# Kernel tuning notes

Hardware: AMD Instinct MI355X
Metric: run time of the kernel (lower is better)

## Reference

```python
import jax, jax.numpy as jnp
import numpy as np

N, F, H, L, E, C = 50000, 256, 64, 8, 1600000, 40
ALPHA, THETA = 0.1, 0.5


def setup_inputs() -> dict:
    key = jax.random.key(0)
    ks = jax.random.split(key, 8)
    x = jax.random.normal(ks[0], (N, F), jnp.float32)
    edge_index = jax.random.randint(ks[1], (2, E), 0, N)
    edge_weight = jax.random.uniform(ks[2], (E,), jnp.float32)
    W0 = jax.random.normal(ks[3], (F, H), jnp.float32) / np.sqrt(F).astype(np.float32)
    b0 = jnp.zeros((H,), jnp.float32)
    Wl = jax.random.normal(ks[4], (L, H, H), jnp.float32) / np.sqrt(H).astype(np.float32)
    W2 = jax.random.normal(ks[5], (H * H, C), jnp.float32) / np.sqrt(H * H).astype(np.float32)
    b2 = jnp.zeros((C,), jnp.float32)
    return dict(x=x, edge_index=edge_index, edge_weight=edge_weight,
                W0=W0, b0=b0, Wl=Wl, W2=W2, b2=b2)


def reference(x, edge_index, edge_weight, W0, b0, Wl, W2, b2):
    src, dst = edge_index[0], edge_index[1]
    # initial projection (dropout p=0.0 is identity)
    h0 = jax.nn.relu(x @ W0 + b0)          # [N, H]
    h = h0
    for l in range(L):
        # GCN2Conv, shared_weights=True, normalize=False
        # SpMM: agg[dst] += w * h[src]
        agg = jax.ops.segment_sum(edge_weight[:, None] * h[src], dst, num_segments=N)
        beta = jnp.float32(np.log(THETA / (l + 1) + 1.0))
        hmix = (1.0 - ALPHA) * agg + ALPHA * h0  # initial residual blend
        h = jax.nn.relu((1.0 - beta) * hmix + beta * (hmix @ Wl[l]))
    # outer-product head: [N,H,H] -> [N, H*H]
    op = jnp.einsum('ni,nj->nij', h, h).reshape(N, H * H)
    logits = op @ W2 + b2                  # [N, C]
    return jax.nn.log_softmax(logits, axis=-1)
```

## Files before the change

kernel.cpp:

```cpp
#include <hip/hip_runtime.h>
#include <hip/hip_bf16.h>
#include <math.h>

#define NN 50000
#define FF 256
#define HH 64
#define LL 8
#define EE 1600000
#define CC 40

#define BK 64
#define NB ((NN + BK - 1) / BK)
#define PBK 4096
#define NPART ((EE + PBK - 1) / PBK)

using short8 = __attribute__((ext_vector_type(8))) short;
using short4v = __attribute__((ext_vector_type(4))) short;
using f32x4  = __attribute__((ext_vector_type(4))) float;

static __device__ __forceinline__ unsigned short f2b(float f) {
    union { __hip_bfloat16 h; unsigned short u; } cv;
    cv.h = __float2bfloat16(f);
    return cv.u;
}
static __device__ __forceinline__ float b2f(unsigned short u) {
    return __uint_as_float((unsigned)u << 16);
}


__global__ void k_hist(const int* __restrict__ dst, int* __restrict__ cnt) {
    int e = blockIdx.x * 256 + threadIdx.x;
    if (e < EE) atomicAdd(&cnt[dst[e]], 1);
}

__global__ void k_scanA(const int* __restrict__ cnt, int* __restrict__ incl, int* __restrict__ bsum) {
    __shared__ int buf[1024];
    int i = blockIdx.x * 1024 + threadIdx.x;
    int v = (i < NN) ? cnt[i] : 0;
    buf[threadIdx.x] = v;
    __syncthreads();
    for (int off = 1; off < 1024; off <<= 1) {
        int t = (threadIdx.x >= off) ? buf[threadIdx.x - off] : 0;
        __syncthreads();
        buf[threadIdx.x] += t;
        __syncthreads();
    }
    if (i < NN) incl[i] = buf[threadIdx.x];
    if (threadIdx.x == 1023) bsum[blockIdx.x] = buf[1023];
}

__global__ void k_scanB(int* __restrict__ bsum) {
    int t = threadIdx.x;
    int vin = (t < 49) ? bsum[t] : 0;
    int v = vin;
    for (int off = 1; off < 64; off <<= 1) {
        int u = __shfl_up(v, off);
        if (t >= off) v += u;
    }
    if (t < 49) bsum[t] = v - vin;
}

__global__ void k_scanC(const int* __restrict__ cnt, const int* __restrict__ incl,
                        const int* __restrict__ bsum, int* __restrict__ row_ptr) {
    int i = blockIdx.x * 1024 + threadIdx.x;
    if (i < NN) row_ptr[i] = incl[i] - cnt[i] + bsum[blockIdx.x];
    if (i == 0) row_ptr[NN] = EE;
}

__global__ void k_binit(const int* __restrict__ row_ptr, int* __restrict__ bcur) {
    int t = blockIdx.x * 256 + threadIdx.x;
    if (t < NB) bcur[t] = row_ptr[t * BK];
}

__global__ void k_part(const int* __restrict__ src, const int* __restrict__ dst,
                       const float* __restrict__ w, int* __restrict__ bcur,
                       uint2* __restrict__ ebuk) {
    __shared__ int lh[NB];
    __shared__ int lbase[NB];
    int t = threadIdx.x;
    int e0 = blockIdx.x * PBK;
    int e1 = min(e0 + PBK, EE);
    for (int i = t; i < NB; i += 256) lh[i] = 0;
    __syncthreads();
    for (int e = e0 + t; e < e1; e += 256)
        atomicAdd(&lh[(unsigned)dst[e] >> 6], 1);
    __syncthreads();
    for (int i = t; i < NB; i += 256) {
        int c = lh[i];
        lbase[i] = c ? atomicAdd(&bcur[i], c) : 0;
    }
    __syncthreads();
    for (int i = t; i < NB; i += 256) lh[i] = 0;
    __syncthreads();
    for (int e = e0 + t; e < e1; e += 256) {
        int d = dst[e];
        int b = (unsigned)d >> 6;
        int r = atomicAdd(&lh[b], 1);
        ebuk[lbase[b] + r] = make_uint2(((unsigned)src[e] << 16) | (unsigned)f2b(w[e]),
                                        (unsigned)d);
    }
}

__global__ void k_sub(const int* __restrict__ row_ptr, const uint2* __restrict__ ebuk,
                      unsigned* __restrict__ pay) {
    __shared__ int lcur[BK];
    int b = blockIdx.x;
    int d0 = b * BK;
    int t = threadIdx.x;
    if (t < BK && d0 + t < NN) lcur[t] = row_ptr[d0 + t];
    __syncthreads();
    int lo = row_ptr[d0];
    int hi = row_ptr[min(d0 + BK, NN)];
    for (int i = lo + t; i < hi; i += 256) {
        uint2 pk = ebuk[i];
        int p = atomicAdd(&lcur[pk.y - d0], 1);
        pay[p] = pk.x;
    }
}

__global__ void k_w2b(const float* __restrict__ W2, unsigned short* __restrict__ W2b) {
    int o = blockIdx.x * 256 + threadIdx.x;
    if (o < 3 * 64 * 16 * 64) {
        int j = o & 63;
        int cr = (o >> 6) & 15;
        int i = (o >> 10) & 63;
        int ct = o >> 16;
        int c = ct * 16 + cr;
        float v = (c < CC) ? W2[((size_t)i * 64 + j) * CC + c] : 0.f;
        W2b[o] = f2b(v);
    }
}

__global__ __launch_bounds__(512) void k_h0m(const float* __restrict__ x,
                                             const float* __restrict__ W0,
                                             const float* __restrict__ b0,
                                             float* __restrict__ h0f,
                                             unsigned short* __restrict__ h0b) {
    __shared__ __align__(16) __hip_bfloat16 ax[256][72];
    __shared__ __align__(16) __hip_bfloat16 bw[64][72];

    int tid = threadIdx.x;
    int lane = tid & 63;
    int w = tid >> 6;
    int nbase = blockIdx.x * 256;

    f32x4 acc[2][4];
#pragma unroll
    for (int nf = 0; nf < 2; ++nf)
#pragma unroll
        for (int cf = 0; cf < 4; ++cf) acc[nf][cf] = (f32x4){0.f, 0.f, 0.f, 0.f};

    int arow = w * 32 + (lane & 15);
    int kq = (lane >> 4) * 8;

    for (int kc = 0; kc < 4; ++kc) {
        __syncthreads();
#pragma unroll
        for (int p = 0; p < 8; ++p) {
            int q = p * 512 + tid;
            int r = q >> 4, cq = q & 15;
            int node = nbase + r;
            float4 v = {0.f, 0.f, 0.f, 0.f};
            if (node < NN) v = *(const float4*)&x[(size_t)node * FF + kc * 64 + cq * 4];
            __hip_bfloat16* d = &ax[r][cq * 4];
            d[0] = __float2bfloat16(v.x);
            d[1] = __float2bfloat16(v.y);
            d[2] = __float2bfloat16(v.z);
            d[3] = __float2bfloat16(v.w);
        }
#pragma unroll
        for (int u = 0; u < 8; ++u) {
            int k = (tid >> 6) * 8 + u;
            float v = W0[(size_t)(kc * 64 + k) * HH + lane];
            bw[lane][k] = __float2bfloat16(v);
        }
        __syncthreads();
#pragma unroll
        for (int ks = 0; ks < 2; ++ks) {
            short8 a0 = *(const short8*)&ax[arow][ks * 32 + kq];
            short8 a1 = *(const short8*)&ax[arow + 16][ks * 32 + kq];
#pragma unroll
            for (int cf = 0; cf < 4; ++cf) {
                short8 b = *(const short8*)&bw[cf * 16 + (lane & 15)][ks * 32 + kq];
                acc[0][cf] = __builtin_amdgcn_mfma_f32_16x16x32_bf16(a0, b, acc[0][cf], 0, 0, 0);
                acc[1][cf] = __builtin_amdgcn_mfma_f32_16x16x32_bf16(a1, b, acc[1][cf], 0, 0, 0);
            }
        }
    }

#pragma unroll
    for (int nf = 0; nf < 2; ++nf) {
#pragma unroll
        for (int cf = 0; cf < 4; ++cf) {
            int c = cf * 16 + (lane & 15);
            float bias = b0[c];
#pragma unroll
            for (int r = 0; r < 4; ++r) {
                int node = nbase + w * 32 + nf * 16 + ((lane >> 4) << 2) + r;
                if (node < NN) {
                    float v = fmaxf(acc[nf][cf][r] + bias, 0.f);
                    h0f[(size_t)node * HH + c] = v;
                    h0b[(size_t)node * HH + c] = f2b(v);
                }
            }
        }
    }
}

__global__ __launch_bounds__(256, 8) void k_layer(
        const unsigned short* __restrict__ hin, const float* __restrict__ h0,
        const int* __restrict__ row_ptr, const unsigned* __restrict__ pay,
        const float* __restrict__ Wl, float beta,
        unsigned short* __restrict__ hout) {
    int lane = threadIdx.x & 63;
    int half = lane >> 5;
    int j = lane & 31;
    int n0 = (blockIdx.x * 4 + (threadIdx.x >> 6)) * 4;

    const unsigned* __restrict__ hin32 = (const unsigned*)hin;

    float hmix[4];
#pragma unroll
    for (int u = 0; u < 4; ++u) {
        int n = n0 + u;
        int rb = row_ptr[n], re = row_ptr[n + 1];
        float ax0 = 0.f, ay0 = 0.f, ax1 = 0.f, ay1 = 0.f;
        for (int base = rb; base < re; base += 64) {
            int idx = base + lane;
            unsigned pv = (idx < re) ? pay[idx] : 0u;
            int ecnt = min(64, re - base);
            for (int k = 0; k < ecnt; k += 8) {
                unsigned pk[8];
#pragma unroll
                for (int t = 0; t < 8; t++)
                    pk[t] = (unsigned)__builtin_amdgcn_readlane((int)pv, k + t);
                unsigned m0 = half ? pk[1] : pk[0];
                unsigned m1 = half ? pk[3] : pk[2];
                unsigned m2 = half ? pk[5] : pk[4];
                unsigned m3 = half ? pk[7] : pk[6];
                unsigned u0 = hin32[(size_t)(m0 >> 16) * 32 + j];
                unsigned u1 = hin32[(size_t)(m1 >> 16) * 32 + j];
                unsigned u2 = hin32[(size_t)(m2 >> 16) * 32 + j];
                unsigned u3 = hin32[(size_t)(m3 >> 16) * 32 + j];
                float w0 = __uint_as_float((m0 & 0xFFFFu) << 16);
                float w1 = __uint_as_float((m1 & 0xFFFFu) << 16);
                float w2 = __uint_as_float((m2 & 0xFFFFu) << 16);
                float w3 = __uint_as_float((m3 & 0xFFFFu) << 16);
                ax0 = fmaf(w0, __uint_as_float(u0 << 16), ax0);
                ay0 = fmaf(w0, __uint_as_float(u0 & 0xFFFF0000u), ay0);
                ax1 = fmaf(w1, __uint_as_float(u1 << 16), ax1);
                ay1 = fmaf(w1, __uint_as_float(u1 & 0xFFFF0000u), ay1);
                ax0 = fmaf(w2, __uint_as_float(u2 << 16), ax0);
                ay0 = fmaf(w2, __uint_as_float(u2 & 0xFFFF0000u), ay0);
                ax1 = fmaf(w3, __uint_as_float(u3 << 16), ax1);
                ay1 = fmaf(w3, __uint_as_float(u3 & 0xFFFF0000u), ay1);
            }
        }
        float ax = ax0 + ax1, ay = ay0 + ay1;
        ax += __shfl_xor(ax, 32);
        ay += __shfl_xor(ay, 32);
        float vx = __shfl(ax, lane >> 1);
        float vy = __shfl(ay, lane >> 1);
        float acc = (lane & 1) ? vy : vx;
        hmix[u] = fmaf(0.9f, acc, 0.1f * h0[(size_t)n * HH + lane]);
    }

    int hb[4];
#pragma unroll
    for (int u = 0; u < 4; ++u) hb[u] = __float_as_int(hmix[u]);
    float a2[4] = {0.f, 0.f, 0.f, 0.f};
#pragma unroll
    for (int jj = 0; jj < HH; jj++) {
        float wr = Wl[jj * HH + lane];
#pragma unroll
        for (int u = 0; u < 4; ++u) {
            float hj = __int_as_float(__builtin_amdgcn_readlane(hb[u], jj));
            a2[u] = fmaf(hj, wr, a2[u]);
        }
    }
#pragma unroll
    for (int u = 0; u < 4; ++u) {
        float outv = (1.f - beta) * hmix[u] + beta * a2[u];
        hout[(size_t)(n0 + u) * HH + lane] = f2b(fmaxf(outv, 0.f));
    }
}

__global__ __launch_bounds__(512) void k_head(const unsigned short* __restrict__ h,
                                              const unsigned short* __restrict__ W2b,
                                              const float* __restrict__ b2,
                                              float* __restrict__ out) {
    __shared__ __align__(16) unsigned short Bl[32 * 1056];

    int tid = threadIdx.x;
    int lane = tid & 63;
    int w = tid >> 6;
    int nbase = blockIdx.x * 256;
    int ct = blockIdx.y;
    int c0 = ct * 16;

    int kq = (lane >> 4) * 8;
    int arow = w * 32 + (lane & 15);
    int rb4 = w * 32 + ((lane >> 4) << 2);

    int ra0 = min(nbase + arow, NN - 1);
    int ra1 = min(nbase + arow + 16, NN - 1);
    short8 af00 = *(const short8*)&h[(size_t)ra0 * HH + kq];
    short8 af01 = *(const short8*)&h[(size_t)ra0 * HH + 32 + kq];
    short8 af10 = *(const short8*)&h[(size_t)ra1 * HH + kq];
    short8 af11 = *(const short8*)&h[(size_t)ra1 * HH + 32 + kq];

    const unsigned short* srow[8];
#pragma unroll
    for (int r = 0; r < 4; ++r) {
        srow[r]     = &h[(size_t)min(nbase + rb4 + r, NN - 1) * HH];
        srow[4 + r] = &h[(size_t)min(nbase + rb4 + 16 + r, NN - 1) * HH];
    }

    const f32x4 zf = (f32x4){0.f, 0.f, 0.f, 0.f};
    f32x4 acc0 = zf, acc1 = zf;

    const unsigned short* __restrict__ Wslice = W2b + (size_t)ct * 65536;

    for (int ph = 0; ph < 2; ++ph) {
        __syncthreads();
        const unsigned short* src = Wslice + (size_t)ph * 32768;
#pragma unroll
        for (int rnd = 0; rnd < 8; ++rnd) {
            int cid = rnd * 512 + tid;
            int il = cid >> 7;
            int rem = cid & 127;
            int cr = rem >> 3;
            int jg = rem & 7;
            *(short8*)&Bl[il * 1056 + cr * 66 + jg * 8] =
                *(const short8*)&src[(size_t)cid * 8];
        }
        __syncthreads();

#pragma unroll
        for (int ihl = 0; ihl < 8; ++ihl) {
            int ibase = ihl * 4;
            int ig = ph * 32 + ibase;
            short8 B00 = *(const short8*)&Bl[(ibase + 0) * 1056 + (lane & 15) * 66 + kq];
            short8 B01 = *(const short8*)&Bl[(ibase + 0) * 1056 + (lane & 15) * 66 + 32 + kq];
            short8 B10 = *(const short8*)&Bl[(ibase + 1) * 1056 + (lane & 15) * 66 + kq];
            short8 B11 = *(const short8*)&Bl[(ibase + 1) * 1056 + (lane & 15) * 66 + 32 + kq];
            short8 B20 = *(const short8*)&Bl[(ibase + 2) * 1056 + (lane & 15) * 66 + kq];
            short8 B21 = *(const short8*)&Bl[(ibase + 2) * 1056 + (lane & 15) * 66 + 32 + kq];
            short8 B30 = *(const short8*)&Bl[(ibase + 3) * 1056 + (lane & 15) * 66 + kq];
            short8 B31 = *(const short8*)&Bl[(ibase + 3) * 1056 + (lane & 15) * 66 + 32 + kq];
            short4v sa0 = *(const short4v*)&srow[0][ig];
            short4v sa1 = *(const short4v*)&srow[1][ig];
            short4v sa2 = *(const short4v*)&srow[2][ig];
            short4v sa3 = *(const short4v*)&srow[3][ig];
            short4v sb0 = *(const short4v*)&srow[4][ig];
            short4v sb1 = *(const short4v*)&srow[5][ig];
            short4v sb2 = *(const short4v*)&srow[6][ig];
            short4v sb3 = *(const short4v*)&srow[7][ig];

#define ILB(IL, B0, B1)                                                          \
            {                                                                    \
                f32x4 t;                                                         \
                t = __builtin_amdgcn_mfma_f32_16x16x32_bf16(af00, B0, zf, 0, 0, 0); \
                t = __builtin_amdgcn_mfma_f32_16x16x32_bf16(af01, B1, t, 0, 0, 0);  \
                acc0[0] = fmaf(b2f((unsigned short)sa0[IL]), t[0], acc0[0]);     \
                acc0[1] = fmaf(b2f((unsigned short)sa1[IL]), t[1], acc0[1]);     \
                acc0[2] = fmaf(b2f((unsigned short)sa2[IL]), t[2], acc0[2]);     \
                acc0[3] = fmaf(b2f((unsigned short)sa3[IL]), t[3], acc0[3]);     \
                t = __builtin_amdgcn_mfma_f32_16x16x32_bf16(af10, B0, zf, 0, 0, 0); \
                t = __builtin_amdgcn_mfma_f32_16x16x32_bf16(af11, B1, t, 0, 0, 0);  \
                acc1[0] = fmaf(b2f((unsigned short)sb0[IL]), t[0], acc1[0]);     \
                acc1[1] = fmaf(b2f((unsigned short)sb1[IL]), t[1], acc1[1]);     \
                acc1[2] = fmaf(b2f((unsigned short)sb2[IL]), t[2], acc1[2]);     \
                acc1[3] = fmaf(b2f((unsigned short)sb3[IL]), t[3], acc1[3]);     \
            }
            ILB(0, B00, B01)
            ILB(1, B10, B11)
            ILB(2, B20, B21)
            ILB(3, B30, B31)
#undef ILB
        }
    }

    int c = c0 + (lane & 15);
    if (c < CC) {
        float bias = b2[c];
#pragma unroll
        for (int r = 0; r < 4; ++r) {
            int node0 = nbase + rb4 + r;
            if (node0 < NN) out[(size_t)node0 * CC + c] = acc0[r] + bias;
            int node1 = nbase + rb4 + 16 + r;
            if (node1 < NN) out[(size_t)node1 * CC + c] = acc1[r] + bias;
        }
    }
}

__global__ void k_lsm(float* __restrict__ out) {
    int lane = threadIdx.x & 63;
    int n = (blockIdx.x * 256 + threadIdx.x) >> 6;
    if (n >= NN) return;
    float x = (lane < CC) ? out[(size_t)n * CC + lane] : -INFINITY;
    float m = x;
    for (int off = 32; off; off >>= 1) m = fmaxf(m, __shfl_xor(m, off));
    float e = (lane < CC) ? expf(x - m) : 0.f;
    float s = e;
    for (int off = 32; off; off >>= 1) s += __shfl_xor(s, off);
    float lse = m + logf(s);
    if (lane < CC) out[(size_t)n * CC + lane] = x - lse;
}

extern "C" void kernel_launch(void* const* d_in, const int* in_sizes, int n_in,
                              void* d_out, int out_size, void* d_ws, size_t ws_size,
                              hipStream_t stream) {
    const float* x  = (const float*)d_in[0];
    const int*   ei = (const int*)d_in[1];
    const float* ew = (const float*)d_in[2];
    const float* W0 = (const float*)d_in[3];
    const float* b0 = (const float*)d_in[4];
    const float* Wl = (const float*)d_in[5];
    const float* W2 = (const float*)d_in[6];
    const float* b2 = (const float*)d_in[7];
    float* out = (float*)d_out;

    char* ws = (char*)d_ws;
    size_t off = 0;
    auto alloc = [&](size_t b) { size_t o = off; off += (b + 255) & ~(size_t)255; return o; };
    float*          h0f = (float*)(ws + alloc((size_t)NN * HH * 4));
    unsigned short* h0b = (unsigned short*)(ws + alloc((size_t)NN * HH * 2));
    unsigned short* hA  = (unsigned short*)(ws + alloc((size_t)NN * HH * 2));
    unsigned short* hB  = (unsigned short*)(ws + alloc((size_t)NN * HH * 2));
    int*      cnt     = (int*)(ws + alloc((size_t)NN * 4));
    int*      incl    = (int*)(ws + alloc((size_t)NN * 4));
    int*      bsum    = (int*)(ws + alloc(256));
    int*      row_ptr = (int*)(ws + alloc((size_t)(NN + 1) * 4));
    int*      bcur    = (int*)(ws + alloc((size_t)NB * 4));
    uint2*    ebuk    = (uint2*)(ws + alloc((size_t)EE * 8));
    unsigned* pay     = (unsigned*)(ws + alloc((size_t)EE * 4));
    unsigned short* W2b = (unsigned short*)(ws + alloc((size_t)3 * 64 * 16 * 64 * 2));

    const int* srcp = ei;
    const int* dstp = ei + EE;

    hipMemsetAsync(cnt, 0, (size_t)NN * 4, stream);
    k_hist<<<(EE + 255) / 256, 256, 0, stream>>>(dstp, cnt);
    k_scanA<<<49, 1024, 0, stream>>>(cnt, incl, bsum);
    k_scanB<<<1, 64, 0, stream>>>(bsum);
    k_scanC<<<49, 1024, 0, stream>>>(cnt, incl, bsum, row_ptr);
    k_binit<<<(NB + 255) / 256, 256, 0, stream>>>(row_ptr, bcur);
    k_part<<<NPART, 256, 0, stream>>>(srcp, dstp, ew, bcur, ebuk);
    k_sub<<<NB, 256, 0, stream>>>(row_ptr, ebuk, pay);
    k_w2b<<<768, 256, 0, stream>>>(W2, W2b);

    k_h0m<<<196, 512, 0, stream>>>(x, W0, b0, h0f, h0b);

    const unsigned short* hin = h0b;
    unsigned short* ho = hA;
    for (int l = 0; l < LL; l++) {
        float beta = (float)log(0.5 / (double)(l + 1) + 1.0);
        k_layer<<<3125, 256, 0, stream>>>(hin, h0f, row_ptr, pay,
                                          Wl + (size_t)l * HH * HH, beta, ho);
        hin = ho;
        ho = (ho == hA) ? hB : hA;
    }

    k_head<<<dim3(196, 3), 512, 0, stream>>>(hin, W2b, b2, out);
    k_lsm<<<(NN * 64 + 255) / 256, 256, 0, stream>>>(out);
}
```

Measured before the change: 536.3 us.

## Build CSR via bucket-level histogram and per-bucket local scan

Replaces the per-node global atomic histogram and the three-pass scan with a block-local shared-memory histogram over 64-node buckets, followed by a single-block scan of the bucket counts. Per-node row pointers are then computed inside k_sub from a local count and a wave scan over each bucket's edges. This removes 1.6M global atomics and several kernel launches, at the cost of k_sub reading the bucket's edges twice.

```diff
diff --git a/kernel.cpp b/kernel.cpp
--- a/kernel.cpp
+++ b/kernel.cpp
@@ -27,49 +27,40 @@
     return __uint_as_float((unsigned)u << 16);
 }
 
-
-__global__ void k_hist(const int* __restrict__ dst, int* __restrict__ cnt) {
-    int e = blockIdx.x * 256 + threadIdx.x;
-    if (e < EE) atomicAdd(&cnt[dst[e]], 1);
-}
-
-__global__ void k_scanA(const int* __restrict__ cnt, int* __restrict__ incl, int* __restrict__ bsum) {
+__global__ void k_bhist(const int* __restrict__ dst, int* __restrict__ bcnt) {
+    __shared__ int lh[NB];
+    int t = threadIdx.x;
+    int e0 = blockIdx.x * PBK;
+    int e1 = min(e0 + PBK, EE);
+    for (int i = t; i < NB; i += 256) lh[i] = 0;
+    __syncthreads();
+    for (int e = e0 + t; e < e1; e += 256)
+        atomicAdd(&lh[(unsigned)dst[e] >> 6], 1);
+    __syncthreads();
+    for (int i = t; i < NB; i += 256)
+        if (lh[i]) atomicAdd(&bcnt[i], lh[i]);
+}
+
+__global__ void k_bscan(const int* __restrict__ bcnt, int* __restrict__ bbase) {
     __shared__ int buf[1024];
-    int i = blockIdx.x * 1024 + threadIdx.x;
-    int v = (i < NN) ? cnt[i] : 0;
-    buf[threadIdx.x] = v;
+    int t = threadIdx.x;
+    int v = (t < NB) ? bcnt[t] : 0;
+    int vin = v;
+    buf[t] = v;
     __syncthreads();
     for (int off = 1; off < 1024; off <<= 1) {
-        int t = (threadIdx.x >= off) ? buf[threadIdx.x - off] : 0;
-        __syncthreads();
-        buf[threadIdx.x] += t;
-        __syncthreads();
-    }
-    if (i < NN) incl[i] = buf[threadIdx.x];
-    if (threadIdx.x == 1023) bsum[blockIdx.x] = buf[1023];
-}
-
-__global__ void k_scanB(int* __restrict__ bsum) {
-    int t = threadIdx.x;
-    int vin = (t < 49) ? bsum[t] : 0;
-    int v = vin;
-    for (int off = 1; off < 64; off <<= 1) {
-        int u = __shfl_up(v, off);
-        if (t >= off) v += u;
-    }
-    if (t < 49) bsum[t] = v - vin;
-}
-
-__global__ void k_scanC(const int* __restrict__ cnt, const int* __restrict__ incl,
-                        const int* __restrict__ bsum, int* __restrict__ row_ptr) {
-    int i = blockIdx.x * 1024 + threadIdx.x;
-    if (i < NN) row_ptr[i] = incl[i] - cnt[i] + bsum[blockIdx.x];
-    if (i == 0) row_ptr[NN] = EE;
-}
-
-__global__ void k_binit(const int* __restrict__ row_ptr, int* __restrict__ bcur) {
+        int u = (t >= off) ? buf[t - off] : 0;
+        __syncthreads();
+        buf[t] += u;
+        __syncthreads();
+    }
+    if (t < NB) bbase[t] = buf[t] - vin;
+    if (t == 0) bbase[NB] = EE;
+}
+
+__global__ void k_binit(const int* __restrict__ bbase, int* __restrict__ bcur) {
     int t = blockIdx.x * 256 + threadIdx.x;
-    if (t < NB) bcur[t] = row_ptr[t * BK];
+    if (t < NB) bcur[t] = bbase[t];
 }
 
 __global__ void k_part(const int* __restrict__ src, const int* __restrict__ dst,
@@ -101,16 +92,33 @@
     }
 }
 
-__global__ void k_sub(const int* __restrict__ row_ptr, const uint2* __restrict__ ebuk,
-                      unsigned* __restrict__ pay) {
+__global__ void k_sub(const int* __restrict__ bbase, const uint2* __restrict__ ebuk,
+                      unsigned* __restrict__ pay, int* __restrict__ row_ptr) {
+    __shared__ int lcnt[BK];
     __shared__ int lcur[BK];
     int b = blockIdx.x;
     int d0 = b * BK;
+    int bksz = min(BK, NN - d0);
     int t = threadIdx.x;
-    if (t < BK && d0 + t < NN) lcur[t] = row_ptr[d0 + t];
-    __syncthreads();
-    int lo = row_ptr[d0];
-    int hi = row_ptr[min(d0 + BK, NN)];
+    if (t < BK) lcnt[t] = 0;
+    __syncthreads();
+    int lo = bbase[b], hi = bbase[b + 1];
+    for (int i = lo + t; i < hi; i += 256)
+        atomicAdd(&lcnt[ebuk[i].y - d0], 1);
+    __syncthreads();
+    if (t < 64) {
+        int vin = lcnt[t];
+        int v = vin;
+        for (int off = 1; off < 64; off <<= 1) {
+            int u = __shfl_up(v, off);
+            if (t >= off) v += u;
+        }
+        int excl = v - vin + lo;
+        lcur[t] = excl;
+        if (t < bksz) row_ptr[d0 + t] = excl;
+    }
+    if (b == NB - 1 && t == 0) row_ptr[NN] = EE;
+    __syncthreads();
     for (int i = lo + t; i < hi; i += 256) {
         uint2 pk = ebuk[i];
         int p = atomicAdd(&lcur[pk.y - d0], 1);
@@ -428,11 +436,10 @@
     unsigned short* h0b = (unsigned short*)(ws + alloc((size_t)NN * HH * 2));
     unsigned short* hA  = (unsigned short*)(ws + alloc((size_t)NN * HH * 2));
     unsigned short* hB  = (unsigned short*)(ws + alloc((size_t)NN * HH * 2));
-    int*      cnt     = (int*)(ws + alloc((size_t)NN * 4));
-    int*      incl    = (int*)(ws + alloc((size_t)NN * 4));
-    int*      bsum    = (int*)(ws + alloc(256));
+    int*      bcnt    = (int*)(ws + alloc((size_t)NB * 4));
+    int*      bbase   = (int*)(ws + alloc((size_t)(NB + 1) * 4));
+    int*      bcur    = (int*)(ws + alloc((size_t)NB * 4));
     int*      row_ptr = (int*)(ws + alloc((size_t)(NN + 1) * 4));
-    int*      bcur    = (int*)(ws + alloc((size_t)NB * 4));
     uint2*    ebuk    = (uint2*)(ws + alloc((size_t)EE * 8));
     unsigned* pay     = (unsigned*)(ws + alloc((size_t)EE * 4));
     unsigned short* W2b = (unsigned short*)(ws + alloc((size_t)3 * 64 * 16 * 64 * 2));
@@ -440,14 +447,12 @@
     const int* srcp = ei;
     const int* dstp = ei + EE;
 
-    hipMemsetAsync(cnt, 0, (size_t)NN * 4, stream);
-    k_hist<<<(EE + 255) / 256, 256, 0, stream>>>(dstp, cnt);
-    k_scanA<<<49, 1024, 0, stream>>>(cnt, incl, bsum);
-    k_scanB<<<1, 64, 0, stream>>>(bsum);
-    k_scanC<<<49, 1024, 0, stream>>>(cnt, incl, bsum, row_ptr);
-    k_binit<<<(NB + 255) / 256, 256, 0, stream>>>(row_ptr, bcur);
+    hipMemsetAsync(bcnt, 0, (size_t)NB * 4, stream);
+    k_bhist<<<NPART, 256, 0, stream>>>(dstp, bcnt);
+    k_bscan<<<1, 1024, 0, stream>>>(bcnt, bbase);
+    k_binit<<<(NB + 255) / 256, 256, 0, stream>>>(bbase, bcur);
     k_part<<<NPART, 256, 0, stream>>>(srcp, dstp, ew, bcur, ebuk);
-    k_sub<<<NB, 256, 0, stream>>>(row_ptr, ebuk, pay);
+    k_sub<<<NB, 256, 0, stream>>>(bbase, ebuk, pay, row_ptr);
     k_w2b<<<768, 256, 0, stream>>>(W2, W2b);
 
     k_h0m<<<196, 512, 0, stream>>>(x, W0, b0, h0f, h0b);
```

Result: faster. 476.2 us (-11.2%).
